# Performance work log

Hardware: AMD Instinct MI355X
Metric: run time of the kernel (lower is better)

Reference implementation:

```python
import jax, jax.numpy as jnp
import numpy as np

D = 512  # internal width hard-coded in the module


def setup_inputs() -> dict:
    key = jax.random.key(0)
    ks = jax.random.split(key, 12)
    B, S, dim1, dim2 = 8, 2048, 768, 1024
    s1 = 1.0 / np.sqrt(dim1)
    s2 = 1.0 / np.sqrt(dim2)
    sd = 1.0 / np.sqrt(D)
    return {
        "x1": jax.random.normal(ks[0], (B, S, dim1), jnp.float32),
        "x2": jax.random.normal(ks[1], (B, S, dim2), jnp.float32),
        "W_p1": jax.random.uniform(ks[2], (dim1, D), jnp.float32, -s1, s1),
        "b_p1": jax.random.uniform(ks[3], (D,), jnp.float32, -s1, s1),
        "W_p2": jax.random.uniform(ks[4], (dim2, D), jnp.float32, -s2, s2),
        "b_p2": jax.random.uniform(ks[5], (D,), jnp.float32, -s2, s2),
        "W_q": jax.random.uniform(ks[6], (D, D), jnp.float32, -sd, sd),
        "b_q": jax.random.uniform(ks[7], (D,), jnp.float32, -sd, sd),
        "W_k": jax.random.uniform(ks[8], (D, D), jnp.float32, -sd, sd),
        "b_k": jax.random.uniform(ks[9], (D,), jnp.float32, -sd, sd),
        "W_v": jax.random.uniform(ks[10], (D, D), jnp.float32, -sd, sd),
        "b_v": jax.random.uniform(ks[11], (D,), jnp.float32, -sd, sd),
        "gamma": jnp.zeros((1,), jnp.float32),
    }


def _attend(q, k, v):
    # q: [B,Sq,D], k/v: [B,Sk,D] -> [B,Sq,D]
    scores = jnp.einsum("bqd,bkd->bqk", q, k) / np.sqrt(D).astype(np.float32)
    w = jax.nn.softmax(scores, axis=-1)
    return jnp.einsum("bqk,bkd->bqd", w, v)


def reference(x1, x2, W_p1, b_p1, W_p2, b_p2, W_q, b_q, W_k, b_k, W_v, b_v, gamma):
    h1 = x1 @ W_p1 + b_p1  # [B,S,512]
    h2 = x2 @ W_p2 + b_p2  # [B,S,512]
    # direction 1: queries from h1, keys/values from h2
    fused1 = _attend(h1 @ W_q + b_q, h2 @ W_k + b_k, h2 @ W_v + b_v)
    # direction 2: queries from h2, keys/values from h1
    fused2 = _attend(h2 @ W_q + b_q, h1 @ W_k + b_k, h1 @ W_v + b_v)
    return gamma * (fused1 + fused2) + h1 + h2
```

## Files before the change

### kernel.cpp

```cpp
#include <hip/hip_runtime.h>
#include <stdint.h>


typedef __bf16 bf16x8 __attribute__((ext_vector_type(8)));
typedef float f32x4 __attribute__((ext_vector_type(4)));
typedef unsigned short u16x8 __attribute__((ext_vector_type(8)));
typedef unsigned short u16x4 __attribute__((ext_vector_type(4)));
typedef unsigned short u16x2 __attribute__((ext_vector_type(2)));

typedef __attribute__((address_space(3))) unsigned int as3_u32;
typedef const __attribute__((address_space(1))) unsigned int as1_u32;

__device__ __forceinline__ float bf2f(unsigned short h) {
  union { unsigned int u; float f; } v; v.u = ((unsigned int)h) << 16; return v.f;
}
__device__ __forceinline__ unsigned short f2bf(float f) {
  union { float f; unsigned int u; } v; v.f = f;
  unsigned int u = v.u;
  return (unsigned short)((u + 0x7fffu + ((u >> 16) & 1u)) >> 16);
}
__device__ __forceinline__ bf16x8 as_bf16x8(u16x8 x) {
  union { u16x8 u; bf16x8 b; } c; c.u = x; return c.b;
}
__device__ __forceinline__ void async_load16(unsigned short* lds, const unsigned short* g) {
  __builtin_amdgcn_global_load_lds((as1_u32*)g, (as3_u32*)lds, 16, 0, 0);
}

__global__ __launch_bounds__(256) void transpose_all_lds(
    const float* __restrict__ Wp1, const float* __restrict__ Wp2,
    const float* __restrict__ Wq, const float* __restrict__ Wk,
    const float* __restrict__ Wv,
    unsigned short* __restrict__ o1, unsigned short* __restrict__ o2,
    unsigned short* __restrict__ oq, unsigned short* __restrict__ ok,
    unsigned short* __restrict__ ov,
    const float* __restrict__ gamma)
{
  __shared__ unsigned short sT[64][72];
  const int bid = blockIdx.x;
  const int tid = threadIdx.x;

  const float* src; unsigned short* dst; int K, ktiles, base;
  if (bid < 96)       { src = Wp1; dst = o1; K = 768;  ktiles = 12; base = 0; }
  else if (bid < 224) { src = Wp2; dst = o2; K = 1024; ktiles = 16; base = 96; }
  else {
    if (gamma[0] == 0.0f) return;
    K = 512; ktiles = 8;
    if (bid < 288)      { src = Wq; dst = oq; base = 224; }
    else if (bid < 352) { src = Wk; dst = ok; base = 288; }
    else                { src = Wv; dst = ov; base = 352; }
  }
  const int local = bid - base;
  const int k0 = (local % ktiles) * 64;
  const int n0 = (local / ktiles) * 64;

  const int rr = tid >> 4, c4 = tid & 15;
#pragma unroll
  for (int i = 0; i < 4; ++i) {
    int row = i * 16 + rr;
    f32x4 v = *(const f32x4*)(src + (size_t)(k0 + row) * 512 + n0 + c4 * 4);
#pragma unroll
    for (int j = 0; j < 4; ++j)
      sT[c4 * 4 + j][row] = f2bf(v[j]);
  }
  __syncthreads();

  const int nr = tid >> 3, kq = tid & 7;
#pragma unroll
  for (int i = 0; i < 2; ++i) {
    int n = i * 32 + nr;
    *(u16x8*)(dst + (size_t)(n0 + n) * K + k0 + kq * 8) = *(const u16x8*)&sT[n][kq * 8];
  }
}

__global__ __launch_bounds__(256, 5) void fused_h12_out(
    const float* __restrict__ x1, const float* __restrict__ x2,
    const unsigned short* __restrict__ WT1, const unsigned short* __restrict__ WT2,
    const float* __restrict__ b1, const float* __restrict__ b2,
    float* __restrict__ out, const float* __restrict__ gamma)
{
  if (gamma[0] != 0.0f) return;
  __shared__ __align__(16) unsigned short sA[2][64 * 64];
  __shared__ __align__(16) unsigned short sB[2][64 * 64];
  const int tid = threadIdx.x;
  const int lane = tid & 63;
  const int w = tid >> 6;
  const int wm = w & 1, wn = w >> 1;
  const int l15 = lane & 15, lg = lane >> 4;

  const int f = blockIdx.x;
  const int bx = f >> 8;
  const int by = f & 255;
  const size_t row0A = (size_t)by * 64;
  const int row0B = bx * 64;

  f32x4 ar[4];
  f32x4 acc[2][2] = {};

  auto loadA = [&](int kk) {
#pragma unroll
    for (int i = 0; i < 4; ++i) {
      int cc = i * 256 + tid;
      int row = cc >> 4, c4 = cc & 15;
      const float* ap = (kk < 768)
          ? (x1 + (row0A + row) * 768 + kk + c4 * 4)
          : (x2 + (row0A + row) * 1024 + (kk - 768) + c4 * 4);
      ar[i] = *(const f32x4*)ap;
    }
  };
  auto stageB = [&](int kk, int buf) {
#pragma unroll
    for (int j = 0; j < 2; ++j) {
      int cc = (w * 2 + j) * 64 + lane;
      int r = cc >> 3, c = cc & 7;
      int cs = c ^ (r & 7);
      const unsigned short* bp = (kk < 768)
          ? (WT1 + (size_t)(row0B + r) * 768 + kk + cs * 8)
          : (WT2 + (size_t)(row0B + r) * 1024 + (kk - 768) + cs * 8);
      async_load16(&sB[buf][(size_t)(w * 2 + j) * 512], bp);
    }
  };
  auto writeA = [&](int buf) {
#pragma unroll
    for (int i = 0; i < 4; ++i) {
      int cc = i * 256 + tid;
      int row = cc >> 4, c4 = cc & 15;
      int c = c4 >> 1, half = c4 & 1;
      u16x4 hv;
#pragma unroll
      for (int j = 0; j < 4; ++j) hv[j] = f2bf(ar[i][j]);
      *(u16x4*)&sA[buf][row * 64 + ((c ^ (row & 7)) << 3) + (half << 2)] = hv;
    }
  };
  auto compute = [&](int buf) {
#pragma unroll
    for (int ks = 0; ks < 2; ++ks) {
      bf16x8 af[2], bfr[2];
#pragma unroll
      for (int mb = 0; mb < 2; ++mb) {
        int row = wm * 32 + mb * 16 + l15;
        int cs = (ks * 4 + lg) ^ (row & 7);
        af[mb] = *(const bf16x8*)&sA[buf][row * 64 + cs * 8];
      }
#pragma unroll
      for (int nb = 0; nb < 2; ++nb) {
        int row = wn * 32 + nb * 16 + l15;
        int cs = (ks * 4 + lg) ^ (row & 7);
        bfr[nb] = *(const bf16x8*)&sB[buf][row * 64 + cs * 8];
      }
#pragma unroll
      for (int mb = 0; mb < 2; ++mb)
#pragma unroll
        for (int nb = 0; nb < 2; ++nb)
          acc[mb][nb] = __builtin_amdgcn_mfma_f32_16x16x32_bf16(af[mb], bfr[nb], acc[mb][nb], 0, 0, 0);
    }
  };

  loadA(0);
  stageB(0, 0);
  writeA(0);
  __syncthreads();

  const int NT = 28;
  int cur = 0;
  for (int t = 0; t < NT; ++t) {
    if (t + 1 < NT) {
      stageB((t + 1) * 64, cur ^ 1);
      loadA((t + 1) * 64);
    }
    compute(cur);
    if (t + 1 < NT) writeA(cur ^ 1);
    __syncthreads();
    cur ^= 1;
  }

  const int colb = row0B + wn * 32;
#pragma unroll
  for (int nb = 0; nb < 2; ++nb) {
    int col = colb + nb * 16 + l15;
    float bv = b1[col] + b2[col];
#pragma unroll
    for (int mb = 0; mb < 2; ++mb) {
      size_t rowb = row0A + wm * 32 + mb * 16 + lg * 4;
#pragma unroll
      for (int r = 0; r < 4; ++r)
        out[(rowb + r) * 512 + col] = acc[mb][nb][r] + bv;
    }
  }
}

__global__ __launch_bounds__(256) void gemm_h12(
    const float* __restrict__ x1, const float* __restrict__ x2,
    const unsigned short* __restrict__ WT1, const unsigned short* __restrict__ WT2,
    const float* __restrict__ b1, const float* __restrict__ b2,
    unsigned short* __restrict__ h1b, unsigned short* __restrict__ h2b,
    const float* __restrict__ gate)
{
  if (gate[0] == 0.0f) return;
  const int z = blockIdx.z;
  const float* A = z ? x2 : x1;
  const unsigned short* Bt = z ? WT2 : WT1;
  const float* bias = z ? b2 : b1;
  unsigned short* C = z ? h2b : h1b;
  const int K = z ? 1024 : 768;
  const int ldc = 512;

  __shared__ __align__(16) unsigned short sA[128 * 32];
  __shared__ __align__(16) unsigned short sB[128 * 32];
  const int tid = threadIdx.x;
  const int lane = tid & 63;
  const int w = tid >> 6;
  const int wm = w & 1, wn = w >> 1;
  const int l15 = lane & 15, lg = lane >> 4;
  const size_t row0A = (size_t)blockIdx.x * 128;
  const size_t row0B = (size_t)blockIdx.y * 128;
  f32x4 acc[4][4] = {};

  for (int kb = 0; kb < K; kb += 32) {
#pragma unroll
    for (int j = 0; j < 2; ++j) {
      int cc = (w * 2 + j) * 64 + lane;
      int r = cc >> 2, k8 = cc & 3;
      async_load16(&sB[(size_t)((w * 2 + j) * 64) * 8], Bt + (row0B + r) * K + kb + k8 * 8);
    }
    {
#pragma unroll
      for (int i = 0; i < 4; ++i) {
        int cc = i * 256 + tid;
        int row = cc >> 3, c4 = cc & 7;
        f32x4 v = *(const f32x4*)(A + (row0A + row) * K + kb + c4 * 4);
        u16x4 hv;
#pragma unroll
        for (int j = 0; j < 4; ++j) hv[j] = f2bf(v[j]);
        *(u16x4*)&sA[row * 32 + c4 * 4] = hv;
      }
    }
    __syncthreads();
    bf16x8 af[4], bfr[4];
#pragma unroll
    for (int mb = 0; mb < 4; ++mb)
      af[mb] = *(const bf16x8*)&sA[(wm * 64 + mb * 16 + l15) * 32 + lg * 8];
#pragma unroll
    for (int nb = 0; nb < 4; ++nb)
      bfr[nb] = *(const bf16x8*)&sB[(wn * 64 + nb * 16 + l15) * 32 + lg * 8];
#pragma unroll
    for (int mb = 0; mb < 4; ++mb)
#pragma unroll
      for (int nb = 0; nb < 4; ++nb)
        acc[mb][nb] = __builtin_amdgcn_mfma_f32_16x16x32_bf16(af[mb], bfr[nb], acc[mb][nb], 0, 0, 0);
    __syncthreads();
  }

  const int colb = (int)row0B + wn * 64;
#pragma unroll
  for (int nb = 0; nb < 4; ++nb) {
    int col = colb + nb * 16 + l15;
    float bv = bias[col];
#pragma unroll
    for (int mb = 0; mb < 4; ++mb) {
      size_t rowb = row0A + wm * 64 + mb * 16 + lg * 4;
#pragma unroll
      for (int r = 0; r < 4; ++r)
        C[(rowb + r) * ldc + col] = f2bf(acc[mb][nb][r] + bv);
    }
  }
}

__global__ __launch_bounds__(256) void gemm_qkv(
    const unsigned short* __restrict__ Aq,
    const unsigned short* __restrict__ Akv,
    const unsigned short* __restrict__ Wq_, const unsigned short* __restrict__ Wk_,
    const unsigned short* __restrict__ Wv_,
    const float* __restrict__ bq_, const float* __restrict__ bk_,
    const float* __restrict__ bv_,
    unsigned short* __restrict__ P,
    const float* __restrict__ gate)
{
  if (gate[0] == 0.0f) return;
  const int z = blockIdx.z;
  const unsigned short* A  = (z == 0) ? Aq : Akv;
  const unsigned short* Bt = (z == 0) ? Wq_ : (z == 1 ? Wk_ : Wv_);
  const float* bias        = (z == 0) ? bq_ : (z == 1 ? bk_ : bv_);
  unsigned short* C = P + z * 512;
  const int K = 512, ldc = 1536;

  __shared__ __align__(16) unsigned short sA[128 * 32];
  __shared__ __align__(16) unsigned short sB[128 * 32];
  const int tid = threadIdx.x;
  const int lane = tid & 63;
  const int w = tid >> 6;
  const int wm = w & 1, wn = w >> 1;
  const int l15 = lane & 15, lg = lane >> 4;
  const size_t row0A = (size_t)blockIdx.x * 128;
  const size_t row0B = (size_t)blockIdx.y * 128;
  f32x4 acc[4][4] = {};

  for (int kb = 0; kb < K; kb += 32) {
#pragma unroll
    for (int j = 0; j < 2; ++j) {
      int cc = (w * 2 + j) * 64 + lane;
      int r = cc >> 2, k8 = cc & 3;
      async_load16(&sA[(size_t)((w * 2 + j) * 64) * 8], A + (row0A + r) * K + kb + k8 * 8);
      async_load16(&sB[(size_t)((w * 2 + j) * 64) * 8], Bt + (row0B + r) * K + kb + k8 * 8);
    }
    __syncthreads();
    bf16x8 af[4], bfr[4];
#pragma unroll
    for (int mb = 0; mb < 4; ++mb)
      af[mb] = *(const bf16x8*)&sA[(wm * 64 + mb * 16 + l15) * 32 + lg * 8];
#pragma unroll
    for (int nb = 0; nb < 4; ++nb)
      bfr[nb] = *(const bf16x8*)&sB[(wn * 64 + nb * 16 + l15) * 32 + lg * 8];
#pragma unroll
    for (int mb = 0; mb < 4; ++mb)
#pragma unroll
      for (int nb = 0; nb < 4; ++nb)
        acc[mb][nb] = __builtin_amdgcn_mfma_f32_16x16x32_bf16(af[mb], bfr[nb], acc[mb][nb], 0, 0, 0);
    __syncthreads();
  }

  const int colb = (int)row0B + wn * 64;
#pragma unroll
  for (int nb = 0; nb < 4; ++nb) {
    int col = colb + nb * 16 + l15;
    float bv = bias[col];
#pragma unroll
    for (int mb = 0; mb < 4; ++mb) {
      size_t rowb = row0A + wm * 64 + mb * 16 + lg * 4;
#pragma unroll
      for (int r = 0; r < 4; ++r)
        C[(rowb + r) * ldc + col] = f2bf(acc[mb][nb][r] + bv);
    }
  }
}

#define LDQ 1536
__global__ __launch_bounds__(256) void flash_attn(
    const unsigned short* __restrict__ P,
    const unsigned short* __restrict__ f1,
    const unsigned short* __restrict__ h1b,
    const unsigned short* __restrict__ h2b,
    const float* __restrict__ gamma,
    unsigned short* __restrict__ f1out,
    float* __restrict__ out32,
    int dir)
{
  const float g0 = gamma[0];
  if (g0 == 0.0f) return;

  __shared__ __align__(16) unsigned short KVs[18432];
  __shared__ __align__(16) float Sred[4608];
  __shared__ __align__(16) unsigned short Pt[1152];
  __shared__ float mstate[32], lstate[32], alpha_s[32];

  const int tid = threadIdx.x;
  const int lane = tid & 63;
  const int w = tid >> 6;
  const int l15 = lane & 15, lg = lane >> 4;
  const int wbase = w * 128;
  const int qt = blockIdx.x;
  const int b = blockIdx.y;
  const size_t qrow0 = (size_t)b * 2048 + (size_t)qt * 32;
  const size_t krow0 = (size_t)b * 2048;

  if (tid < 32) { mstate[tid] = -1e30f; lstate[tid] = 0.f; }
  __syncthreads();

  bf16x8 qf[2][4];
#pragma unroll
  for (int mb = 0; mb < 2; ++mb)
#pragma unroll
    for (int ks = 0; ks < 4; ++ks)
      qf[mb][ks] = *(const bf16x8*)(P + (qrow0 + mb * 16 + l15) * LDQ + wbase + ks * 32 + lg * 8);

  f32x4 o[2][8] = {};

  const int srow = tid >> 3, ssub = tid & 7;
  const int kvp = tid & 15, dg = tid >> 4;

  for (int kt = 0; kt < 64; ++kt) {
    const size_t kvb = krow0 + (size_t)kt * 32;
#pragma unroll
    for (int i = 0; i < 8; ++i) {
      int cc = tid + i * 256;
      int r = cc >> 6, c8 = cc & 63;
      *(u16x8*)&KVs[r * 520 + c8 * 8] = *(const u16x8*)(P + (kvb + r) * LDQ + 512 + c8 * 8);
    }
    __syncthreads();

    f32x4 sacc[2][2] = {};
#pragma unroll
    for (int ks = 0; ks < 4; ++ks)
#pragma unroll
      for (int nb = 0; nb < 2; ++nb) {
        bf16x8 kf = *(const bf16x8*)&KVs[(nb * 16 + l15) * 520 + wbase + ks * 32 + lg * 8];
#pragma unroll
        for (int mb = 0; mb < 2; ++mb)
          sacc[mb][nb] = __builtin_amdgcn_mfma_f32_16x16x32_bf16(qf[mb][ks], kf, sacc[mb][nb], 0, 0, 0);
      }
#pragma unroll
    for (int mb = 0; mb < 2; ++mb)
#pragma unroll
      for (int nb = 0; nb < 2; ++nb)
#pragma unroll
        for (int r = 0; r < 4; ++r)
          Sred[w * 1152 + (mb * 16 + lg * 4 + r) * 36 + nb * 16 + l15] = sacc[mb][nb][r];
    __syncthreads();

    {
      f32x4 sv = {};
#pragma unroll
      for (int w2 = 0; w2 < 4; ++w2)
        sv += *(const f32x4*)&Sred[w2 * 1152 + srow * 36 + ssub * 4];
      const float scale = 0.044194173824159216f;
      sv *= scale;
      float mloc = fmaxf(fmaxf(sv[0], sv[1]), fmaxf(sv[2], sv[3]));
      mloc = fmaxf(mloc, __shfl_xor(mloc, 1));
      mloc = fmaxf(mloc, __shfl_xor(mloc, 2));
      mloc = fmaxf(mloc, __shfl_xor(mloc, 4));
      float mold = mstate[srow];
      float mnew = fmaxf(mold, mloc);
      const float LOG2E = 1.4426950408889634f;
      float p0 = exp2f((sv[0] - mnew) * LOG2E);
      float p1 = exp2f((sv[1] - mnew) * LOG2E);
      float p2 = exp2f((sv[2] - mnew) * LOG2E);
      float p3 = exp2f((sv[3] - mnew) * LOG2E);
      float lloc = p0 + p1 + p2 + p3;
      lloc += __shfl_xor(lloc, 1);
      lloc += __shfl_xor(lloc, 2);
      lloc += __shfl_xor(lloc, 4);
      float alpha = exp2f((mold - mnew) * LOG2E);
      if (ssub == 0) {
        mstate[srow] = mnew;
        lstate[srow] = lstate[srow] * alpha + lloc;
        alpha_s[srow] = alpha;
      }
      u16x4 pw;
      pw[0] = f2bf(p0); pw[1] = f2bf(p1); pw[2] = f2bf(p2); pw[3] = f2bf(p3);
      *(u16x4*)&Pt[srow * 36 + ssub * 4] = pw;
    }
#pragma unroll
    for (int i = 0; i < 4; ++i) {
      int d0 = (dg + i * 16) * 8;
      u16x8 v0 = *(const u16x8*)(P + (kvb + kvp * 2) * LDQ + 1024 + d0);
      u16x8 v1 = *(const u16x8*)(P + (kvb + kvp * 2 + 1) * LDQ + 1024 + d0);
#pragma unroll
      for (int j = 0; j < 8; ++j) {
        u16x2 t2; t2[0] = v0[j]; t2[1] = v1[j];
        *(u16x2*)&KVs[(d0 + j) * 36 + kvp * 2] = t2;
      }
    }
    __syncthreads();

    float al[2][4];
#pragma unroll
    for (int mb = 0; mb < 2; ++mb)
#pragma unroll
      for (int r = 0; r < 4; ++r)
        al[mb][r] = alpha_s[mb * 16 + lg * 4 + r];
#pragma unroll
    for (int mb = 0; mb < 2; ++mb)
#pragma unroll
      for (int nb = 0; nb < 8; ++nb)
#pragma unroll
        for (int r = 0; r < 4; ++r)
          o[mb][nb][r] *= al[mb][r];

    bf16x8 pf[2];
#pragma unroll
    for (int mb = 0; mb < 2; ++mb) {
      u16x4 lo = *(const u16x4*)&Pt[(mb * 16 + l15) * 36 + lg * 8];
      u16x4 hi = *(const u16x4*)&Pt[(mb * 16 + l15) * 36 + lg * 8 + 4];
      pf[mb] = as_bf16x8(__builtin_shufflevector(lo, hi, 0, 1, 2, 3, 4, 5, 6, 7));
    }
#pragma unroll
    for (int nb = 0; nb < 8; ++nb) {
      int d = wbase + nb * 16 + l15;
      u16x4 lo = *(const u16x4*)&KVs[d * 36 + lg * 8];
      u16x4 hi = *(const u16x4*)&KVs[d * 36 + lg * 8 + 4];
      bf16x8 vf = as_bf16x8(__builtin_shufflevector(lo, hi, 0, 1, 2, 3, 4, 5, 6, 7));
#pragma unroll
      for (int mb = 0; mb < 2; ++mb)
        o[mb][nb] = __builtin_amdgcn_mfma_f32_16x16x32_bf16(pf[mb], vf, o[mb][nb], 0, 0, 0);
    }
    __syncthreads();
  }

  float li[2][4];
#pragma unroll
  for (int mb = 0; mb < 2; ++mb)
#pragma unroll
    for (int r = 0; r < 4; ++r)
      li[mb][r] = 1.0f / lstate[mb * 16 + lg * 4 + r];

  if (dir == 0) {
#pragma unroll
    for (int mb = 0; mb < 2; ++mb)
#pragma unroll
      for (int nb = 0; nb < 8; ++nb)
#pragma unroll
        for (int r = 0; r < 4; ++r)
          f1out[(qrow0 + mb * 16 + lg * 4 + r) * 512 + wbase + nb * 16 + l15] =
              f2bf(o[mb][nb][r] * li[mb][r]);
  } else {
    float g = g0;
#pragma unroll
    for (int mb = 0; mb < 2; ++mb)
#pragma unroll
      for (int nb = 0; nb < 8; ++nb)
#pragma unroll
        for (int r = 0; r < 4; ++r) {
          size_t idx = (qrow0 + mb * 16 + lg * 4 + r) * 512 + wbase + nb * 16 + l15;
          float f1v = bf2f(f1[idx]);
          float f2v = o[mb][nb][r] * li[mb][r];
          out32[idx] = g * (f1v + f2v) + bf2f(h1b[idx]) + bf2f(h2b[idx]);
        }
  }
}

extern "C" void kernel_launch(void* const* d_in, const int* in_sizes, int n_in,
                              void* d_out, int out_size, void* d_ws, size_t ws_size,
                              hipStream_t stream)
{
  const float* x1    = (const float*)d_in[0];
  const float* x2    = (const float*)d_in[1];
  const float* Wp1   = (const float*)d_in[2];
  const float* bp1   = (const float*)d_in[3];
  const float* Wp2   = (const float*)d_in[4];
  const float* bp2   = (const float*)d_in[5];
  const float* Wq    = (const float*)d_in[6];
  const float* bq    = (const float*)d_in[7];
  const float* Wk    = (const float*)d_in[8];
  const float* bk    = (const float*)d_in[9];
  const float* Wv    = (const float*)d_in[10];
  const float* bv    = (const float*)d_in[11];
  const float* gamma = (const float*)d_in[12];
  float* out = (float*)d_out;
  char* ws = (char*)d_ws;

  unsigned short* WTp1 = (unsigned short*)(ws + 0);
  unsigned short* WTp2 = (unsigned short*)(ws + 786432);
  unsigned short* WTq  = (unsigned short*)(ws + 1835008);
  unsigned short* WTk  = (unsigned short*)(ws + 2359296);
  unsigned short* WTv  = (unsigned short*)(ws + 2883584);
  unsigned short* h1b  = (unsigned short*)(ws + 3407872);
  unsigned short* h2b  = (unsigned short*)(ws + 20185088);
  unsigned short* f1b  = (unsigned short*)(ws + 36962304);
  unsigned short* P1   = (unsigned short*)(ws + 53739520);

  transpose_all_lds<<<416, 256, 0, stream>>>(Wp1, Wp2, Wq, Wk, Wv,
                                             WTp1, WTp2, WTq, WTk, WTv, gamma);

  fused_h12_out<<<2048, 256, 0, stream>>>(x1, x2, WTp1, WTp2, bp1, bp2, out, gamma);

  gemm_h12<<<dim3(128, 4, 2), 256, 0, stream>>>(x1, x2, WTp1, WTp2, bp1, bp2, h1b, h2b, gamma);

  gemm_qkv<<<dim3(128, 4, 3), 256, 0, stream>>>(h1b, h2b, WTq, WTk, WTv, bq, bk, bv, P1, gamma);
  flash_attn<<<dim3(64, 8), 256, 0, stream>>>(P1, f1b, h1b, h2b, gamma, f1b, out, 0);

  gemm_qkv<<<dim3(128, 4, 3), 256, 0, stream>>>(h2b, h1b, WTq, WTk, WTv, bq, bk, bv, P1, gamma);
  flash_attn<<<dim3(64, 8), 256, 0, stream>>>(P1, f1b, h1b, h2b, gamma, f1b, out, 1);
}
```

Measured before the change: 231.9 us.

## Pre-convert activations to bf16 and remap grid for A-tile reuse

Extends the transpose kernel with extra blocks that convert x1 and x2 to bf16 in workspace when gamma is zero. The fused projection GEMM then stages A tiles with async global-to-LDS loads, like B, instead of loading fp32 into registers and converting. The block index mapping also changes so the 8 column blocks sharing an A row tile run next to each other, which should improve cache reuse of A. The cost is an extra full conversion pass that reads the fp32 activations and writes bf16 copies, and the copies reuse workspace regions that are otherwise only needed when gamma is non-zero.

```diff
diff --git a/kernel.cpp b/kernel.cpp
--- a/kernel.cpp
+++ b/kernel.cpp
@@ -30,15 +30,32 @@
     const float* __restrict__ Wp1, const float* __restrict__ Wp2,
     const float* __restrict__ Wq, const float* __restrict__ Wk,
     const float* __restrict__ Wv,
+    const float* __restrict__ x1, const float* __restrict__ x2,
     unsigned short* __restrict__ o1, unsigned short* __restrict__ o2,
     unsigned short* __restrict__ oq, unsigned short* __restrict__ ok,
     unsigned short* __restrict__ ov,
+    unsigned short* __restrict__ xbf1, unsigned short* __restrict__ xbf2,
     const float* __restrict__ gamma)
 {
-  __shared__ unsigned short sT[64][72];
   const int bid = blockIdx.x;
   const int tid = threadIdx.x;
 
+  if (bid >= 416) {
+    if (gamma[0] != 0.0f) return;
+    const float* src; unsigned short* dst; int local;
+    if (bid < 6560) { src = x1; dst = xbf1; local = bid - 416; }
+    else            { src = x2; dst = xbf2; local = bid - 6560; }
+    size_t base = (size_t)local * 2048 + (size_t)tid * 8;
+    f32x4 a = *(const f32x4*)(src + base);
+    f32x4 b = *(const f32x4*)(src + base + 4);
+    u16x8 o;
+#pragma unroll
+    for (int j = 0; j < 4; ++j) { o[j] = f2bf(a[j]); o[4 + j] = f2bf(b[j]); }
+    *(u16x8*)(dst + base) = o;
+    return;
+  }
+
+  __shared__ unsigned short sT[64][72];
   const float* src; unsigned short* dst; int K, ktiles, base;
   if (bid < 96)       { src = Wp1; dst = o1; K = 768;  ktiles = 12; base = 0; }
   else if (bid < 224) { src = Wp2; dst = o2; K = 1024; ktiles = 16; base = 96; }
@@ -73,7 +90,7 @@
 }
 
 __global__ __launch_bounds__(256, 5) void fused_h12_out(
-    const float* __restrict__ x1, const float* __restrict__ x2,
+    const unsigned short* __restrict__ xbf1, const unsigned short* __restrict__ xbf2,
     const unsigned short* __restrict__ WT1, const unsigned short* __restrict__ WT2,
     const float* __restrict__ b1, const float* __restrict__ b2,
     float* __restrict__ out, const float* __restrict__ gamma)
@@ -88,23 +105,23 @@
   const int l15 = lane & 15, lg = lane >> 4;
 
   const int f = blockIdx.x;
-  const int bx = f >> 8;
-  const int by = f & 255;
+  const int bx = f & 7;
+  const int by = f >> 3;
   const size_t row0A = (size_t)by * 64;
   const int row0B = bx * 64;
 
-  f32x4 ar[4];
   f32x4 acc[2][2] = {};
 
-  auto loadA = [&](int kk) {
-#pragma unroll
-    for (int i = 0; i < 4; ++i) {
-      int cc = i * 256 + tid;
-      int row = cc >> 4, c4 = cc & 15;
-      const float* ap = (kk < 768)
-          ? (x1 + (row0A + row) * 768 + kk + c4 * 4)
-          : (x2 + (row0A + row) * 1024 + (kk - 768) + c4 * 4);
-      ar[i] = *(const f32x4*)ap;
+  auto stageA = [&](int kk, int buf) {
+#pragma unroll
+    for (int j = 0; j < 2; ++j) {
+      int cc = (w * 2 + j) * 64 + lane;
+      int r = cc >> 3, c = cc & 7;
+      int cs = c ^ (r & 7);
+      const unsigned short* ap = (kk < 768)
+          ? (xbf1 + (size_t)(row0A + r) * 768 + kk + cs * 8)
+          : (xbf2 + (size_t)(row0A + r) * 1024 + (kk - 768) + cs * 8);
+      async_load16(&sA[buf][(size_t)(w * 2 + j) * 512], ap);
     }
   };
   auto stageB = [&](int kk, int buf) {
@@ -119,18 +136,6 @@
       async_load16(&sB[buf][(size_t)(w * 2 + j) * 512], bp);
     }
   };
-  auto writeA = [&](int buf) {
-#pragma unroll
-    for (int i = 0; i < 4; ++i) {
-      int cc = i * 256 + tid;
-      int row = cc >> 4, c4 = cc & 15;
-      int c = c4 >> 1, half = c4 & 1;
-      u16x4 hv;
-#pragma unroll
-      for (int j = 0; j < 4; ++j) hv[j] = f2bf(ar[i][j]);
-      *(u16x4*)&sA[buf][row * 64 + ((c ^ (row & 7)) << 3) + (half << 2)] = hv;
-    }
-  };
   auto compute = [&](int buf) {
 #pragma unroll
     for (int ks = 0; ks < 2; ++ks) {
@@ -155,20 +160,18 @@
     }
   };
 
-  loadA(0);
+  stageA(0, 0);
   stageB(0, 0);
-  writeA(0);
   __syncthreads();
 
   const int NT = 28;
   int cur = 0;
   for (int t = 0; t < NT; ++t) {
     if (t + 1 < NT) {
+      stageA((t + 1) * 64, cur ^ 1);
       stageB((t + 1) * 64, cur ^ 1);
-      loadA((t + 1) * 64);
     }
     compute(cur);
-    if (t + 1 < NT) writeA(cur ^ 1);
     __syncthreads();
     cur ^= 1;
   }
@@ -546,11 +549,14 @@
   unsigned short* h2b  = (unsigned short*)(ws + 20185088);
   unsigned short* f1b  = (unsigned short*)(ws + 36962304);
   unsigned short* P1   = (unsigned short*)(ws + 53739520);
-
-  transpose_all_lds<<<416, 256, 0, stream>>>(Wp1, Wp2, Wq, Wk, Wv,
-                                             WTp1, WTp2, WTq, WTk, WTv, gamma);
-
-  fused_h12_out<<<2048, 256, 0, stream>>>(x1, x2, WTp1, WTp2, bp1, bp2, out, gamma);
+  unsigned short* xbf1 = (unsigned short*)(ws + 3407872);
+  unsigned short* xbf2 = (unsigned short*)(ws + 28573696);
+
+  transpose_all_lds<<<14752, 256, 0, stream>>>(Wp1, Wp2, Wq, Wk, Wv, x1, x2,
+                                               WTp1, WTp2, WTq, WTk, WTv,
+                                               xbf1, xbf2, gamma);
+
+  fused_h12_out<<<2048, 256, 0, stream>>>(xbf1, xbf2, WTp1, WTp2, bp1, bp2, out, gamma);
 
   gemm_h12<<<dim3(128, 4, 2), 256, 0, stream>>>(x1, x2, WTp1, WTp2, bp1, bp2, h1b, h2b, gamma);
 
```

Result: slower. 247.9 us (+6.9%).
